# Optimization experiments

Hardware: AMD Instinct MI355X
Metric: run time of the kernel (lower is better)

Reference implementation:

```python
import jax, jax.numpy as jnp
import numpy as np

N, C, F, T = 8, 4, 257, 2000
B = 8            # spatial_filters (beams)
M = 80           # spectra_filters
EPS = 1e-5


def setup_inputs() -> dict:
    key = jax.random.key(0)
    ks = jax.random.split(key, 10)
    scale = 0.1
    return {
        "x_real": jax.random.normal(ks[0], (N, C, F, T), jnp.float32),
        "x_imag": jax.random.normal(ks[1], (N, C, F, T), jnp.float32),
        # query beamformer (1 beam): conv weights per bin, shape (F, 1, C)
        "wq_r": jax.random.normal(ks[2], (F, 1, C), jnp.float32) * scale,
        "wq_i": jax.random.normal(ks[3], (F, 1, C), jnp.float32) * scale,
        # key/value beamformers: (F, B, C)
        "wk_r": jax.random.normal(ks[4], (F, B, C), jnp.float32) * scale,
        "wk_i": jax.random.normal(ks[5], (F, B, C), jnp.float32) * scale,
        "wv_r": jax.random.normal(ks[6], (F, B, C), jnp.float32) * scale,
        "wv_i": jax.random.normal(ks[7], (F, B, C), jnp.float32) * scale,
        # spectra projection Linear(F -> M, bias=False): torch weight (M, F)
        "proj_w": jax.random.normal(ks[8], (M, F), jnp.float32) * (1.0 / np.sqrt(F)),
        # BatchNorm1d(M) affine params
        "bn_gamma": jnp.ones((M,), jnp.float32),
        "bn_beta": jnp.zeros((M,), jnp.float32),
    }


def _complex_beam_abs(xr, xi, wr, wi):
    # xr/xi: (N,T,F,C); wr/wi: (F,Beams,C)
    # grouped per-bin conv with kernel==length reduces to contraction over C
    rr = jnp.einsum("ntfc,fbc->ntfb", xr, wr)
    ii = jnp.einsum("ntfc,fbc->ntfb", xi, wi)
    ri = jnp.einsum("ntfc,fbc->ntfb", xi, wr)
    ir = jnp.einsum("ntfc,fbc->ntfb", xr, wi)
    br = rr - ii
    bi = ri + ir
    return jnp.sqrt(br * br + bi * bi + EPS)


def reference(x_real, x_imag, wq_r, wq_i, wk_r, wk_i, wv_r, wv_i, proj_w, bn_gamma, bn_beta):
    # N,C,F,T -> N,T,F,C
    xr = jnp.transpose(x_real, (0, 3, 2, 1))
    xi = jnp.transpose(x_imag, (0, 3, 2, 1))
    bq = _complex_beam_abs(xr, xi, wq_r, wq_i)[..., 0]   # (N,T,F)
    bk = _complex_beam_abs(xr, xi, wk_r, wk_i)           # (N,T,F,B)
    bv = _complex_beam_abs(xr, xi, wv_r, wv_i)           # (N,T,F,B)
    s = jnp.sum(bq[..., None] * bk, axis=-2)             # (N,T,B)
    s = jnp.mean(s, axis=-2, keepdims=True)              # (N,1,B) time-invariant
    w = jax.nn.softmax(s, axis=-1)                       # (N,1,B)
    v = jnp.sum(w[:, None] * bv, axis=-1)                # (N,T,F)
    f = jax.nn.relu(jnp.einsum("ntf,mf->ntm", v, proj_w))
    f = jnp.log(f + EPS)                                 # (N,T,M)
    # BatchNorm1d over channel dim M, training-mode batch stats (biased var)
    mu = jnp.mean(f, axis=(0, 1))
    var = jnp.var(f, axis=(0, 1))
    f = (f - mu) * jax.lax.rsqrt(var + EPS) * bn_gamma + bn_beta
    return f
```

## Files before the change

kernel.cpp:

```cpp
#include <hip/hip_runtime.h>
#include <math.h>

#define NN 8
#define CC 4
#define FF 257
#define TT 2000
#define BB 8
#define MM 80
#define EPSF 1e-5f
#define VSTR 260
#define T4N 500

typedef float v2f __attribute__((ext_vector_type(2)));

__device__ __forceinline__ float fsqrt_fast(float x) { return __builtin_amdgcn_sqrtf(x); }
__device__ __forceinline__ float flog_fast(float x)  { return __builtin_amdgcn_logf(x) * 0.69314718055994531f; }
__device__ __forceinline__ v2f sqrt2(v2f m) {
    v2f r; r.x = __builtin_amdgcn_sqrtf(m.x); r.y = __builtin_amdgcn_sqrtf(m.y); return r;
}

__global__ __launch_bounds__(256) void k_beam_s(
    const float* __restrict__ xr_g, const float* __restrict__ xi_g,
    const float* __restrict__ wq_r, const float* __restrict__ wq_i,
    const float* __restrict__ wk_r, const float* __restrict__ wk_i,
    float* __restrict__ s_buf)
{
    int nf = blockIdx.x;
    int n = nf / FF, f = nf % FF;
    int t4 = blockIdx.y * 256 + threadIdx.x;

    float part[BB];
#pragma unroll
    for (int b = 0; b < BB; ++b) part[b] = 0.f;

    if (t4 < T4N) {
        const float* xr_base = xr_g + ((size_t)(n*CC)*FF + f) * TT + t4*4;
        const float* xi_base = xi_g + ((size_t)(n*CC)*FF + f) * TT + t4*4;
        v2f xr2[CC][2], xi2[CC][2];
#pragma unroll
        for (int c = 0; c < CC; ++c) {
            float4 r4 = *reinterpret_cast<const float4*>(xr_base + (size_t)c*FF*TT);
            float4 i4 = *reinterpret_cast<const float4*>(xi_base + (size_t)c*FF*TT);
            xr2[c][0].x = r4.x; xr2[c][0].y = r4.y; xr2[c][1].x = r4.z; xr2[c][1].y = r4.w;
            xi2[c][0].x = i4.x; xi2[c][0].y = i4.y; xi2[c][1].x = i4.z; xi2[c][1].y = i4.w;
        }

        const float4 qr4 = *reinterpret_cast<const float4*>(&wq_r[f*CC]);
        const float4 qi4 = *reinterpret_cast<const float4*>(&wq_i[f*CC]);

        v2f qq[2];
#pragma unroll
        for (int p = 0; p < 2; ++p) {
            v2f qr = xr2[0][p]*qr4.x + xr2[1][p]*qr4.y + xr2[2][p]*qr4.z + xr2[3][p]*qr4.w
                   - xi2[0][p]*qi4.x - xi2[1][p]*qi4.y - xi2[2][p]*qi4.z - xi2[3][p]*qi4.w;
            v2f qi = xi2[0][p]*qr4.x + xi2[1][p]*qr4.y + xi2[2][p]*qr4.z + xi2[3][p]*qr4.w
                   + xr2[0][p]*qi4.x + xr2[1][p]*qi4.y + xr2[2][p]*qi4.z + xr2[3][p]*qi4.w;
            qq[p] = qr*qr + qi*qi + EPSF;
        }

#pragma unroll
        for (int b = 0; b < BB; ++b) {
            const float4 wr4 = *reinterpret_cast<const float4*>(&wk_r[(f*BB + b)*CC]);
            const float4 wi4 = *reinterpret_cast<const float4*>(&wk_i[(f*BB + b)*CC]);
            v2f acc; acc.x = 0.f; acc.y = 0.f;
#pragma unroll
            for (int p = 0; p < 2; ++p) {
                v2f kr = xr2[0][p]*wr4.x + xr2[1][p]*wr4.y + xr2[2][p]*wr4.z + xr2[3][p]*wr4.w
                       - xi2[0][p]*wi4.x - xi2[1][p]*wi4.y - xi2[2][p]*wi4.z - xi2[3][p]*wi4.w;
                v2f ki = xi2[0][p]*wr4.x + xi2[1][p]*wr4.y + xi2[2][p]*wr4.z + xi2[3][p]*wr4.w
                       + xr2[0][p]*wi4.x + xr2[1][p]*wi4.y + xr2[2][p]*wi4.z + xr2[3][p]*wi4.w;
                v2f kk = kr*kr + ki*ki + EPSF;
                acc += sqrt2(qq[p] * kk);
            }
            part[b] = acc.x + acc.y;
        }
    }

    __shared__ float red[4][BB];
    int lane = threadIdx.x & 63, wv = threadIdx.x >> 6;
#pragma unroll
    for (int b = 0; b < BB; ++b) {
        float v = part[b];
#pragma unroll
        for (int m = 32; m >= 1; m >>= 1) v += __shfl_xor(v, m);
        if (lane == 0) red[wv][b] = v;
    }
    __syncthreads();
    if (threadIdx.x < BB) {
        float v = red[0][threadIdx.x] + red[1][threadIdx.x]
                + red[2][threadIdx.x] + red[3][threadIdx.x];
        int bin = (blockIdx.x * 2 + blockIdx.y) & 15;
        atomicAdd(&s_buf[bin*64 + n*BB + threadIdx.x], v);
    }
}

__global__ void k_softmax(const float* __restrict__ s_buf, float* __restrict__ w_buf)
{
    int tid = threadIdx.x;
    if (tid < NN*BB) {
        float v = 0.f;
#pragma unroll
        for (int j = 0; j < 16; ++j) v += s_buf[j*64 + tid];
        v *= (1.0f / TT);
        float mx = v;
#pragma unroll
        for (int m = 4; m >= 1; m >>= 1) mx = fmaxf(mx, __shfl_xor(mx, m));
        float e = expf(v - mx);
        float sm = e;
#pragma unroll
        for (int m = 4; m >= 1; m >>= 1) sm += __shfl_xor(sm, m);
        w_buf[tid] = e / sm;
    }
}

__global__ void k_prep(const float* __restrict__ proj_w, float* __restrict__ proj_pad)
{
    int i = blockIdx.x * 256 + threadIdx.x;
    if (i < MM * 260) {
        int m = i / 260, f = i % 260;
        proj_pad[i] = (f < FF) ? proj_w[m*FF + f] : 0.f;
    }
}

__global__ __launch_bounds__(256) void k_vproj(
    const float* __restrict__ xr_g, const float* __restrict__ xi_g,
    const float* __restrict__ wv_r, const float* __restrict__ wv_i,
    const float* __restrict__ w_buf, const float* __restrict__ proj_pad,
    float* __restrict__ out, double* __restrict__ bn_sum, double* __restrict__ bn_sumsq)
{
    __shared__ float v_lds[16 * VSTR];
    int n = blockIdx.x, chunk = blockIdx.y;
    int t0 = chunk * 16;
    int tid = threadIdx.x;

    float wn[BB];
#pragma unroll
    for (int b = 0; b < BB; ++b) wn[b] = w_buf[n*BB + b];

    if (tid < 64 && (tid & 3) < 3) {
        int t = tid >> 2, f = FF + (tid & 3);
        v_lds[t*VSTR + f] = 0.f;
    }

    int t4s = tid & 3;
    int fbase = tid >> 2;

#pragma unroll 1
    for (int k = 0; k < 4; ++k) {
        int f = fbase + 64*k;
        v2f xr2[CC][2], xi2[CC][2];
#pragma unroll
        for (int c = 0; c < CC; ++c) {
            size_t base = ((size_t)(n*CC + c)*FF + f)*TT + t0 + t4s*4;
            float4 r4 = *reinterpret_cast<const float4*>(xr_g + base);
            float4 i4 = *reinterpret_cast<const float4*>(xi_g + base);
            xr2[c][0].x = r4.x; xr2[c][0].y = r4.y; xr2[c][1].x = r4.z; xr2[c][1].y = r4.w;
            xi2[c][0].x = i4.x; xi2[c][0].y = i4.y; xi2[c][1].x = i4.z; xi2[c][1].y = i4.w;
        }

        v2f vo[2];
        vo[0].x = 0.f; vo[0].y = 0.f; vo[1].x = 0.f; vo[1].y = 0.f;
#pragma unroll
        for (int b = 0; b < BB; ++b) {
            const float4 wr4 = *reinterpret_cast<const float4*>(&wv_r[(f*BB + b)*CC]);
            const float4 wi4 = *reinterpret_cast<const float4*>(&wv_i[(f*BB + b)*CC]);
#pragma unroll
            for (int p = 0; p < 2; ++p) {
                v2f vr = xr2[0][p]*wr4.x + xr2[1][p]*wr4.y + xr2[2][p]*wr4.z + xr2[3][p]*wr4.w
                       - xi2[0][p]*wi4.x - xi2[1][p]*wi4.y - xi2[2][p]*wi4.z - xi2[3][p]*wi4.w;
                v2f vi = xi2[0][p]*wr4.x + xi2[1][p]*wr4.y + xi2[2][p]*wr4.z + xi2[3][p]*wr4.w
                       + xr2[0][p]*wi4.x + xr2[1][p]*wi4.y + xr2[2][p]*wi4.z + xr2[3][p]*wi4.w;
                vo[p] += wn[b] * sqrt2(vr*vr + vi*vi + EPSF);
            }
        }
        v_lds[(t4s*4 + 0)*VSTR + f] = vo[0].x;
        v_lds[(t4s*4 + 1)*VSTR + f] = vo[0].y;
        v_lds[(t4s*4 + 2)*VSTR + f] = vo[1].x;
        v_lds[(t4s*4 + 3)*VSTR + f] = vo[1].y;
    }

    if (tid < 16) {
        int t = t0 + tid;
        float xr[CC], xi[CC];
#pragma unroll
        for (int c = 0; c < CC; ++c) {
            size_t base = ((size_t)(n*CC + c)*FF + 256)*TT + t;
            xr[c] = xr_g[base];
            xi[c] = xi_g[base];
        }
        float v = 0.f;
#pragma unroll
        for (int b = 0; b < BB; ++b) {
            const float4 wr4 = *reinterpret_cast<const float4*>(&wv_r[(256*BB + b)*CC]);
            const float4 wi4 = *reinterpret_cast<const float4*>(&wv_i[(256*BB + b)*CC]);
            float vr = xr[0]*wr4.x + xr[1]*wr4.y + xr[2]*wr4.z + xr[3]*wr4.w
                     - xi[0]*wi4.x - xi[1]*wi4.y - xi[2]*wi4.z - xi[3]*wi4.w;
            float vi = xi[0]*wr4.x + xi[1]*wr4.y + xi[2]*wr4.z + xi[3]*wr4.w
                     + xr[0]*wi4.x + xr[1]*wi4.y + xr[2]*wi4.z + xr[3]*wi4.w;
            v += wn[b] * fsqrt_fast(vr*vr + vi*vi + EPSF);
        }
        v_lds[tid*VSTR + 256] = v;
    }
    __syncthreads();

    int tl = tid & 15, fg = tid >> 4;
    v2f acc2[5];
#pragma unroll
    for (int j = 0; j < 5; ++j) { acc2[j].x = 0.f; acc2[j].y = 0.f; }
    const float* pp = proj_pad + fg * 5 * 260;
#pragma unroll 4
    for (int f4 = 0; f4 < 260; f4 += 4) {
        float4 vv = *reinterpret_cast<const float4*>(&v_lds[tl*VSTR + f4]);
        v2f v0, v1;
        v0.x = vv.x; v0.y = vv.y; v1.x = vv.z; v1.y = vv.w;
#pragma unroll
        for (int j = 0; j < 5; ++j) {
            float4 p = *reinterpret_cast<const float4*>(&pp[j*260 + f4]);
            v2f p0, p1; p0.x = p.x; p0.y = p.y; p1.x = p.z; p1.y = p.w;
            acc2[j] += v0*p0 + v1*p1;
        }
    }

    int t = t0 + tl;
    int bin = chunk & 15;
#pragma unroll
    for (int j = 0; j < 5; ++j) {
        int m = fg*5 + j;
        float r = flog_fast(fmaxf(acc2[j].x + acc2[j].y, 0.f) + EPSF);
        float s1 = r, s2 = r*r;
#pragma unroll
        for (int msk = 8; msk >= 1; msk >>= 1) {
            s1 += __shfl_xor(s1, msk);
            s2 += __shfl_xor(s2, msk);
        }
        out[((size_t)n*TT + t)*MM + m] = r;
        if (tl == 0) {
            atomicAdd(&bn_sum[bin*MM + m], (double)s1);
            atomicAdd(&bn_sumsq[bin*MM + m], (double)s2);
        }
    }
}

__global__ void k_bnprep(const double* __restrict__ bn_sum, const double* __restrict__ bn_sumsq,
                         const float* __restrict__ gamma, const float* __restrict__ beta,
                         float* __restrict__ scale, float* __restrict__ shift)
{
    int m = threadIdx.x;
    if (m < MM) {
        double s = 0.0, q = 0.0;
#pragma unroll
        for (int j = 0; j < 16; ++j) { s += bn_sum[j*MM + m]; q += bn_sumsq[j*MM + m]; }
        double inv = 1.0 / (double)(NN * TT);
        double mu = s * inv;
        double var = q * inv - mu * mu;
        float sc = gamma[m] * rsqrtf((float)var + EPSF);
        scale[m] = sc;
        shift[m] = beta[m] - (float)mu * sc;
    }
}

__global__ __launch_bounds__(256) void k_bnapply(float* __restrict__ out,
                                                 const float* __restrict__ scale,
                                                 const float* __restrict__ shift)
{
    int i4 = blockIdx.x * 256 + threadIdx.x;
    if (i4 < NN*TT*MM/4) {
        float4 v = *reinterpret_cast<const float4*>(&out[i4*4]);
        int m = (i4*4) % MM;
        v.x = v.x*scale[m+0] + shift[m+0];
        v.y = v.y*scale[m+1] + shift[m+1];
        v.z = v.z*scale[m+2] + shift[m+2];
        v.w = v.w*scale[m+3] + shift[m+3];
        *reinterpret_cast<float4*>(&out[i4*4]) = v;
    }
}

extern "C" void kernel_launch(void* const* d_in, const int* in_sizes, int n_in,
                              void* d_out, int out_size, void* d_ws, size_t ws_size,
                              hipStream_t stream)
{
    const float* x_real   = (const float*)d_in[0];
    const float* x_imag   = (const float*)d_in[1];
    const float* wq_r     = (const float*)d_in[2];
    const float* wq_i     = (const float*)d_in[3];
    const float* wk_r     = (const float*)d_in[4];
    const float* wk_i     = (const float*)d_in[5];
    const float* wv_r     = (const float*)d_in[6];
    const float* wv_i     = (const float*)d_in[7];
    const float* proj_w   = (const float*)d_in[8];
    const float* bn_gamma = (const float*)d_in[9];
    const float* bn_beta  = (const float*)d_in[10];
    float* out = (float*)d_out;

    char* ws = (char*)d_ws;
    float*  s_buf    = (float*)(ws + 0);
    float*  w_buf    = (float*)(ws + 4096);
    float*  scale    = (float*)(ws + 4352);
    float*  shift    = (float*)(ws + 4672);
    double* bn_sum   = (double*)(ws + 8192);
    double* bn_sumsq = (double*)(ws + 18432);
    float*  proj_pad = (float*)(ws + 28672);

    hipMemsetAsync(d_ws, 0, 28672, stream);

    k_prep<<<(MM*260 + 255)/256, 256, 0, stream>>>(proj_w, proj_pad);

    dim3 g1(NN*FF, 2);
    k_beam_s<<<g1, 256, 0, stream>>>(x_real, x_imag, wq_r, wq_i, wk_r, wk_i, s_buf);

    k_softmax<<<1, 64, 0, stream>>>(s_buf, w_buf);

    dim3 g3(NN, 125);
    k_vproj<<<g3, 256, 0, stream>>>(x_real, x_imag, wv_r, wv_i, w_buf, proj_pad,
                                    out, bn_sum, bn_sumsq);

    k_bnprep<<<1, 128, 0, stream>>>(bn_sum, bn_sumsq, bn_gamma, bn_beta, scale, shift);

    k_bnapply<<<(NN*TT*MM/4 + 255)/256, 256, 0, stream>>>(out, scale, shift);
}
```

Before: 110.5 us.

## Process two time chunks per block with software-pipelined loads over projection

Each k_vproj block now handles two 16-frame chunks with a double-buffered LDS tile. It issues all of the first chunk's x loads up front, then prefetches the second chunk's inputs while the first chunk's projection runs, so global-load latency overlaps the projection compute. The grid shrinks from 125 to 63 blocks per batch. The extra prefetch registers raise register use, and the smaller grid leaves fewer blocks to spread across CUs.

```diff
diff --git a/kernel.cpp b/kernel.cpp
--- a/kernel.cpp
+++ b/kernel.cpp
@@ -122,42 +122,41 @@
     }
 }
 
-__global__ __launch_bounds__(256) void k_vproj(
+
+__device__ __forceinline__ void load_half(
     const float* __restrict__ xr_g, const float* __restrict__ xi_g,
-    const float* __restrict__ wv_r, const float* __restrict__ wv_i,
-    const float* __restrict__ w_buf, const float* __restrict__ proj_pad,
-    float* __restrict__ out, double* __restrict__ bn_sum, double* __restrict__ bn_sumsq)
-{
-    __shared__ float v_lds[16 * VSTR];
-    int n = blockIdx.x, chunk = blockIdx.y;
-    int t0 = chunk * 16;
-    int tid = threadIdx.x;
-
-    float wn[BB];
-#pragma unroll
-    for (int b = 0; b < BB; ++b) wn[b] = w_buf[n*BB + b];
-
-    if (tid < 64 && (tid & 3) < 3) {
-        int t = tid >> 2, f = FF + (tid & 3);
-        v_lds[t*VSTR + f] = 0.f;
-    }
-
-    int t4s = tid & 3;
-    int fbase = tid >> 2;
-
-#pragma unroll 1
-    for (int k = 0; k < 4; ++k) {
-        int f = fbase + 64*k;
-        v2f xr2[CC][2], xi2[CC][2];
+    int n, int t0, int t4s, int fbase, int k0,
+    float4 (&r)[2][CC], float4 (&im)[2][CC])
+{
+#pragma unroll
+    for (int kk = 0; kk < 2; ++kk) {
+        int f = fbase + 64*(k0 + kk);
 #pragma unroll
         for (int c = 0; c < CC; ++c) {
             size_t base = ((size_t)(n*CC + c)*FF + f)*TT + t0 + t4s*4;
-            float4 r4 = *reinterpret_cast<const float4*>(xr_g + base);
-            float4 i4 = *reinterpret_cast<const float4*>(xi_g + base);
-            xr2[c][0].x = r4.x; xr2[c][0].y = r4.y; xr2[c][1].x = r4.z; xr2[c][1].y = r4.w;
-            xi2[c][0].x = i4.x; xi2[c][0].y = i4.y; xi2[c][1].x = i4.z; xi2[c][1].y = i4.w;
-        }
-
+            r[kk][c]  = *reinterpret_cast<const float4*>(xr_g + base);
+            im[kk][c] = *reinterpret_cast<const float4*>(xi_g + base);
+        }
+    }
+}
+
+__device__ __forceinline__ void fill_half(
+    float* v_lds,
+    const float* __restrict__ wv_r, const float* __restrict__ wv_i,
+    const float (&wn)[BB], int t4s, int fbase, int k0,
+    const float4 (&r)[2][CC], const float4 (&im)[2][CC])
+{
+#pragma unroll
+    for (int kk = 0; kk < 2; ++kk) {
+        int f = fbase + 64*(k0 + kk);
+        v2f xr2[CC][2], xi2[CC][2];
+#pragma unroll
+        for (int c = 0; c < CC; ++c) {
+            xr2[c][0].x = r[kk][c].x;  xr2[c][0].y = r[kk][c].y;
+            xr2[c][1].x = r[kk][c].z;  xr2[c][1].y = r[kk][c].w;
+            xi2[c][0].x = im[kk][c].x; xi2[c][0].y = im[kk][c].y;
+            xi2[c][1].x = im[kk][c].z; xi2[c][1].y = im[kk][c].w;
+        }
         v2f vo[2];
         vo[0].x = 0.f; vo[0].y = 0.f; vo[1].x = 0.f; vo[1].y = 0.f;
 #pragma unroll
@@ -178,31 +177,43 @@
         v_lds[(t4s*4 + 2)*VSTR + f] = vo[1].x;
         v_lds[(t4s*4 + 3)*VSTR + f] = vo[1].y;
     }
-
-    if (tid < 16) {
-        int t = t0 + tid;
-        float xr[CC], xi[CC];
-#pragma unroll
-        for (int c = 0; c < CC; ++c) {
-            size_t base = ((size_t)(n*CC + c)*FF + 256)*TT + t;
-            xr[c] = xr_g[base];
-            xi[c] = xi_g[base];
-        }
-        float v = 0.f;
-#pragma unroll
-        for (int b = 0; b < BB; ++b) {
-            const float4 wr4 = *reinterpret_cast<const float4*>(&wv_r[(256*BB + b)*CC]);
-            const float4 wi4 = *reinterpret_cast<const float4*>(&wv_i[(256*BB + b)*CC]);
-            float vr = xr[0]*wr4.x + xr[1]*wr4.y + xr[2]*wr4.z + xr[3]*wr4.w
-                     - xi[0]*wi4.x - xi[1]*wi4.y - xi[2]*wi4.z - xi[3]*wi4.w;
-            float vi = xi[0]*wr4.x + xi[1]*wr4.y + xi[2]*wr4.z + xi[3]*wr4.w
-                     + xr[0]*wi4.x + xr[1]*wi4.y + xr[2]*wi4.z + xr[3]*wi4.w;
-            v += wn[b] * fsqrt_fast(vr*vr + vi*vi + EPSF);
-        }
-        v_lds[tid*VSTR + 256] = v;
-    }
-    __syncthreads();
-
+}
+
+__device__ __forceinline__ void load_f256(
+    const float* __restrict__ xr_g, const float* __restrict__ xi_g,
+    int n, int t0, int tid, float (&xr)[CC], float (&xi)[CC])
+{
+#pragma unroll
+    for (int c = 0; c < CC; ++c) {
+        size_t base = ((size_t)(n*CC + c)*FF + 256)*TT + t0 + tid;
+        xr[c] = xr_g[base];
+        xi[c] = xi_g[base];
+    }
+}
+
+__device__ __forceinline__ void fill_f256(
+    float* v_lds, const float* __restrict__ wv_r, const float* __restrict__ wv_i,
+    const float (&wn)[BB], int tid, const float (&xr)[CC], const float (&xi)[CC])
+{
+    float v = 0.f;
+#pragma unroll
+    for (int b = 0; b < BB; ++b) {
+        const float4 wr4 = *reinterpret_cast<const float4*>(&wv_r[(256*BB + b)*CC]);
+        const float4 wi4 = *reinterpret_cast<const float4*>(&wv_i[(256*BB + b)*CC]);
+        float vr = xr[0]*wr4.x + xr[1]*wr4.y + xr[2]*wr4.z + xr[3]*wr4.w
+                 - xi[0]*wi4.x - xi[1]*wi4.y - xi[2]*wi4.z - xi[3]*wi4.w;
+        float vi = xi[0]*wr4.x + xi[1]*wr4.y + xi[2]*wr4.z + xi[3]*wr4.w
+                 + xr[0]*wi4.x + xr[1]*wi4.y + xr[2]*wi4.z + xr[3]*wi4.w;
+        v += wn[b] * fsqrt_fast(vr*vr + vi*vi + EPSF);
+    }
+    v_lds[tid*VSTR + 256] = v;
+}
+
+__device__ __forceinline__ void proj_stage(
+    const float* v_lds, const float* __restrict__ proj_pad,
+    float* __restrict__ out, double* __restrict__ bn_sum, double* __restrict__ bn_sumsq,
+    int n, int t0, int bin, int tid)
+{
     int tl = tid & 15, fg = tid >> 4;
     v2f acc2[5];
 #pragma unroll
@@ -222,7 +233,6 @@
     }
 
     int t = t0 + tl;
-    int bin = chunk & 15;
 #pragma unroll
     for (int j = 0; j < 5; ++j) {
         int m = fg*5 + j;
@@ -238,6 +248,61 @@
             atomicAdd(&bn_sum[bin*MM + m], (double)s1);
             atomicAdd(&bn_sumsq[bin*MM + m], (double)s2);
         }
+    }
+}
+
+__global__ __launch_bounds__(256) void k_vproj(
+    const float* __restrict__ xr_g, const float* __restrict__ xi_g,
+    const float* __restrict__ wv_r, const float* __restrict__ wv_i,
+    const float* __restrict__ w_buf, const float* __restrict__ proj_pad,
+    float* __restrict__ out, double* __restrict__ bn_sum, double* __restrict__ bn_sumsq)
+{
+    __shared__ float v_lds[2][16 * VSTR];
+    int n = blockIdx.x;
+    int c0 = blockIdx.y * 2;
+    int c1 = c0 + 1;
+    bool hasB = (c1 < 125);
+    int t0A = c0 * 16, t0B = c1 * 16;
+    int tid = threadIdx.x;
+    int t4s = tid & 3;
+    int fbase = tid >> 2;
+
+    float wn[BB];
+#pragma unroll
+    for (int b = 0; b < BB; ++b) wn[b] = w_buf[n*BB + b];
+
+    if (tid < 64 && (tid & 3) < 3) {
+        int t = tid >> 2, f = FF + (tid & 3);
+        v_lds[0][t*VSTR + f] = 0.f;
+        v_lds[1][t*VSTR + f] = 0.f;
+    }
+
+    float4 r0[2][CC], i0[2][CC], r1[2][CC], i1[2][CC];
+    float xr256[CC], xi256[CC];
+    load_half(xr_g, xi_g, n, t0A, t4s, fbase, 0, r0, i0);
+    load_half(xr_g, xi_g, n, t0A, t4s, fbase, 2, r1, i1);
+    if (tid < 16) load_f256(xr_g, xi_g, n, t0A, tid, xr256, xi256);
+
+    fill_half(v_lds[0], wv_r, wv_i, wn, t4s, fbase, 0, r0, i0);
+    fill_half(v_lds[0], wv_r, wv_i, wn, t4s, fbase, 2, r1, i1);
+    if (tid < 16) fill_f256(v_lds[0], wv_r, wv_i, wn, tid, xr256, xi256);
+    __syncthreads();
+
+    if (hasB) {
+        load_half(xr_g, xi_g, n, t0B, t4s, fbase, 0, r0, i0);
+        if (tid < 16) load_f256(xr_g, xi_g, n, t0B, tid, xr256, xi256);
+    }
+    asm volatile("" ::: "memory");
+
+    proj_stage(v_lds[0], proj_pad, out, bn_sum, bn_sumsq, n, t0A, c0 & 15, tid);
+
+    if (hasB) {
+        load_half(xr_g, xi_g, n, t0B, t4s, fbase, 2, r1, i1);
+        fill_half(v_lds[1], wv_r, wv_i, wn, t4s, fbase, 0, r0, i0);
+        fill_half(v_lds[1], wv_r, wv_i, wn, t4s, fbase, 2, r1, i1);
+        if (tid < 16) fill_f256(v_lds[1], wv_r, wv_i, wn, tid, xr256, xi256);
+        __syncthreads();
+        proj_stage(v_lds[1], proj_pad, out, bn_sum, bn_sumsq, n, t0B, c1 & 15, tid);
     }
 }
 
@@ -310,7 +375,7 @@
 
     k_softmax<<<1, 64, 0, stream>>>(s_buf, w_buf);
 
-    dim3 g3(NN, 125);
+    dim3 g3(NN, 63);
     k_vproj<<<g3, 256, 0, stream>>>(x_real, x_imag, wv_r, wv_i, w_buf, proj_pad,
                                     out, bn_sum, bn_sumsq);
 
```

Result: slower. 129.9 us (+17.5%).
